# Optimization experiments

Hardware: AMD Instinct MI355X
Metric: run time of the kernel (lower is better)

The kernel has to match this reference:

```python
import jax, jax.numpy as jnp
import numpy as np

RMS_EPS = 1.1920928955078125e-07  # torch.finfo(float32).eps, nn.RMSNorm default when eps=None


def setup_inputs() -> dict:
    key = jax.random.key(0)
    ks = jax.random.split(key, 7)
    B, T, C, Wh, E, K = 8, 4096, 256, 1024, 8, 2
    return {
        "x": jax.random.normal(ks[0], (B, T, C), dtype=jnp.float32),
        "rms_weight": jnp.ones((C,), dtype=jnp.float32),
        "W1": jax.random.normal(ks[1], (E, C, Wh), dtype=jnp.float32),
        "b1": jax.random.normal(ks[2], (E, Wh), dtype=jnp.float32),
        "W2": jax.random.normal(ks[3], (E, Wh, C), dtype=jnp.float32),
        "b2": jax.random.normal(ks[4], (E, C), dtype=jnp.float32),
        "expert_ids": jax.random.randint(ks[5], (B, T, K), 0, E, dtype=jnp.int64),
    }


def reference(x, rms_weight, W1, b1, W2, b2, expert_ids):
    # RMSNorm over last dim (torch nn.RMSNorm, eps = float32 eps)
    xn = x * jax.lax.rsqrt(jnp.mean(x * x, axis=-1, keepdims=True) + RMS_EPS) * rms_weight
    # Per-expert 2-layer MLP. The torch code gathers per-token weight copies then bmm's;
    # mathematically identical (and far cheaper in memory) is: run every expert densely,
    # then gather the K selected expert outputs per token.
    h = jax.nn.gelu(jnp.einsum("btc,ecw->btew", xn, W1) + b1, approximate=False)  # [B,T,E,Wh]
    y = jnp.einsum("btew,ewc->btec", h, W2) + b2  # [B,T,E,C]
    # gather selected experts: [B,T,K,C]; dropout p is 0.0 (eval) -> identity
    out = jnp.take_along_axis(y, expert_ids[..., None], axis=2)
    return out
```

## Files before the change

kernel.cpp:

```cpp
#include <hip/hip_runtime.h>
#include <cstdint>

typedef unsigned short ushort_t;
typedef __bf16 bf16x8 __attribute__((ext_vector_type(8)));
typedef ushort_t u16x8 __attribute__((ext_vector_type(8)));
typedef float f32x4 __attribute__((ext_vector_type(4)));
typedef uint32_t u32x4 __attribute__((ext_vector_type(4)));

#define RMS_EPS 1.1920928955078125e-07f

__device__ __forceinline__ ushort_t f2bf(float f) {
  uint32_t u = __builtin_bit_cast(uint32_t, f);
  u += 0x7fffu + ((u >> 16) & 1u);
  return (ushort_t)(u >> 16);
}

__device__ __forceinline__ void g2l16(const ushort_t* g, ushort_t* l) {
  __builtin_amdgcn_global_load_lds(
      (const __attribute__((address_space(1))) uint32_t*)g,
      (__attribute__((address_space(3))) uint32_t*)l, 16, 0, 0);
}

__device__ __forceinline__ f32x4 mfma32(bf16x8 a, bf16x8 b, f32x4 c) {
  return __builtin_amdgcn_mfma_f32_16x16x32_bf16(a, b, c, 0, 0, 0);
}

__device__ __forceinline__ float gelu1(float v) {
  float v2 = v * v;
  float u_ = (0.044715f * v2) * v + v;
  float tq = __expf(-1.5957691216057308f * u_);
  return v * __builtin_amdgcn_rcpf(1.0f + tq);
}

__global__ void rmsnorm_cast(const float* __restrict__ x, const float* __restrict__ w,
                             ushort_t* __restrict__ xn) {
  int token = blockIdx.x * 4 + (threadIdx.x >> 6);
  int lane = threadIdx.x & 63;
  const float4* row = reinterpret_cast<const float4*>(x + (size_t)token * 256);
  float4 v = row[lane];
  float s = v.x * v.x + v.y * v.y + v.z * v.z + v.w * v.w;
#pragma unroll
  for (int off = 1; off < 64; off <<= 1) s += __shfl_xor(s, off);
  float inv = rsqrtf(s * (1.0f / 256.0f) + RMS_EPS);
  const float4* wr = reinterpret_cast<const float4*>(w);
  float4 wv = wr[lane];
  ushort4 o;
  o.x = f2bf(v.x * inv * wv.x);
  o.y = f2bf(v.y * inv * wv.y);
  o.z = f2bf(v.z * inv * wv.z);
  o.w = f2bf(v.w * inv * wv.w);
  *reinterpret_cast<ushort4*>(xn + (size_t)token * 256 + lane * 4) = o;
}

__global__ __launch_bounds__(256) void pack_w(const float* __restrict__ W1,
                                              const float* __restrict__ W2,
                                              ushort_t* __restrict__ w1f,
                                              ushort_t* __restrict__ w2f) {
  __shared__ ushort_t tile[64][130];
  int b = blockIdx.x;
  int isW2 = b >= 256;
  const float* src; ushort_t* dst; int e, kt, wt, rs;
  if (!isW2) { e = b >> 5; kt = (b >> 3) & 3; wt = b & 7; src = W1; dst = w1f; rs = 1024; }
  else { b -= 256; e = b >> 5; kt = (b >> 1) & 15; wt = b & 1; src = W2; dst = w2f; rs = 256; }
  int k0 = kt * 64, c0 = wt * 128;
  const float* sb = src + ((size_t)e << 18) + (size_t)k0 * rs + c0;
  int t = threadIdx.x;
#pragma unroll
  for (int i = 0; i < 8; ++i) {
    int f = i * 1024 + t * 4;
    int r = f >> 7, c = f & 127;
    float4 v = *reinterpret_cast<const float4*>(sb + (size_t)r * rs + c);
    ushort2 lo, hi;
    lo.x = f2bf(v.x); lo.y = f2bf(v.y); hi.x = f2bf(v.z); hi.y = f2bf(v.w);
    *reinterpret_cast<ushort2*>(&tile[r][c]) = lo;
    *reinterpret_cast<ushort2*>(&tile[r][c + 2]) = hi;
  }
  __syncthreads();
  int lane = t & 63, l16 = lane & 15, quad = lane >> 4;
  int wave = t >> 6;
  if (!isW2) {
#pragma unroll
    for (int p = 0; p < 4; ++p) {
      int u = p * 256 + t;
      int kk2 = (u >> 9) & 1;
      int rr = kk2 * 32 + quad * 8;
      int nt = (u >> 6) & 1, chL = (u >> 7) & 3;
      int cc = chL * 32 + nt * 16 + l16;
      u16x8 o;
#pragma unroll
      for (int j = 0; j < 8; ++j) o[j] = tile[rr + j][cc];
      size_t U = ((size_t)e * 32768) + (size_t)(wt * 4 + chL) * 1024 + (kt * 2 + kk2) * 128 + nt * 64 + lane;
      *reinterpret_cast<u16x8*>(dst + U * 8) = o;
    }
  } else {
#pragma unroll
    for (int p = 0; p < 4; ++p) {
      int u = p * 4 + wave;
      int chL = u >> 3, ctL = u & 7;
      int cc = ctL * 16 + l16;
      u16x8 o;
#pragma unroll
      for (int j = 0; j < 4; ++j) o[j] = tile[chL * 32 + quad * 4 + j][cc];
#pragma unroll
      for (int j = 0; j < 4; ++j) o[4 + j] = tile[chL * 32 + 16 + quad * 4 + j][cc];
      size_t U = (((size_t)(e * 32 + kt * 2 + chL) * 16) + (wt * 8 + ctL)) * 64 + lane;
      *reinterpret_cast<u16x8*>(dst + U * 8) = o;
    }
  }
}

__global__ void route_pairs(const int* __restrict__ eids, int* __restrict__ cnt,
                            int* __restrict__ lists) {
  __shared__ int lcnt[8], lbase[8];
  int tid = threadIdx.x;
  if (tid < 8) lcnt[tid] = 0;
  __syncthreads();
  int p = blockIdx.x * 256 + tid;
  int e = eids[p];
  int lpos = atomicAdd(&lcnt[e], 1);
  __syncthreads();
  if (tid < 8) lbase[tid] = atomicAdd(&cnt[tid], lcnt[tid]);
  __syncthreads();
  lists[e * 65536 + lbase[e] + lpos] = p;
}

__global__ __launch_bounds__(256, 2) void moe_mlp(
    const ushort_t* __restrict__ xn,
    const ushort_t* __restrict__ w1f,
    const ushort_t* __restrict__ w2f,
    const float* __restrict__ b1,
    const float* __restrict__ b2,
    const int* __restrict__ cnt,
    const int* __restrict__ lists,
    float* __restrict__ out)
{
  __shared__ __align__(16) ushort_t w1b[2][8192];
  __shared__ __align__(16) ushort_t w2b[8192];

  int flat = blockIdx.x;
  int e = -1, tile = 0, accum = 0, n_e = 0;
#pragma unroll
  for (int i = 0; i < 8; ++i) {
    int c = cnt[i];
    int t = (c + 127) >> 7;
    if (e < 0 && flat < accum + t) { e = i; tile = flat - accum; n_e = c; }
    accum += t;
  }
  if (e < 0) return;
  int start = tile * 128;

  int tid = threadIdx.x;
  int wave = tid >> 6, lane = tid & 63, l16 = lane & 15, quad = lane >> 4;

  const ushort_t* w1e = w1f + ((size_t)e << 18);
  const ushort_t* w2e = w2f + ((size_t)e << 18);
  const int* le = lists + e * 65536;

  int gi0 = start + wave * 32 + l16;
  int gi1 = gi0 + 16;
  int pr0 = le[(gi0 < n_e) ? gi0 : 0];
  int pr1 = le[(gi1 < n_e) ? gi1 : 0];

#pragma unroll
  for (int j = 0; j < 4; ++j) {
    int p = j * 4 + wave;
    g2l16(w1e + p * 512 + lane * 8, &w1b[0][p * 512]);
  }

  bf16x8 afr[2][8];
  {
    const u32x4* ar0 = reinterpret_cast<const u32x4*>(xn + (size_t)(pr0 >> 1) * 256);
    const u32x4* ar1 = reinterpret_cast<const u32x4*>(xn + (size_t)(pr1 >> 1) * 256);
#pragma unroll
    for (int kk = 0; kk < 8; ++kk) {
      afr[0][kk] = __builtin_bit_cast(bf16x8, ar0[kk * 4 + quad]);
      afr[1][kk] = __builtin_bit_cast(bf16x8, ar1[kk * 4 + quad]);
    }
  }

  f32x4 acc[2][16];
#pragma unroll
  for (int mt = 0; mt < 2; ++mt)
#pragma unroll
    for (int ct = 0; ct < 16; ++ct) acc[mt][ct] = (f32x4){0.f, 0.f, 0.f, 0.f};

  const float* b1e = b1 + e * 1024;

  for (int ch = 0; ch < 32; ++ch) {
    int cur = ch & 1;
    __syncthreads();

    {
      const ushort_t* n2 = w2e + ch * 8192;
#pragma unroll
      for (int j = 0; j < 4; ++j) {
        int p = j * 4 + wave;
        g2l16(n2 + p * 512 + lane * 8, &w2b[p * 512]);
      }
    }
    if (ch + 1 < 32) {
      const ushort_t* n1 = w1e + (ch + 1) * 8192;
#pragma unroll
      for (int j = 0; j < 4; ++j) {
        int p = j * 4 + wave;
        g2l16(n1 + p * 512 + lane * 8, &w1b[cur ^ 1][p * 512]);
      }
    }

    int w0 = ch * 32;
    f32x4 bia0 = *reinterpret_cast<const f32x4*>(b1e + w0 + quad * 4);
    f32x4 bia1 = *reinterpret_cast<const f32x4*>(b1e + w0 + 16 + quad * 4);

    const ushort_t* l1 = w1b[cur];
    f32x4 ht00 = (f32x4){0.f, 0.f, 0.f, 0.f};
    f32x4 ht01 = (f32x4){0.f, 0.f, 0.f, 0.f};
    f32x4 ht10 = (f32x4){0.f, 0.f, 0.f, 0.f};
    f32x4 ht11 = (f32x4){0.f, 0.f, 0.f, 0.f};
#pragma unroll
    for (int kk = 0; kk < 8; ++kk) {
      bf16x8 wA = *reinterpret_cast<const bf16x8*>(l1 + ((kk * 2 + 0) * 64 + lane) * 8);
      bf16x8 wB = *reinterpret_cast<const bf16x8*>(l1 + ((kk * 2 + 1) * 64 + lane) * 8);
      ht00 = mfma32(wA, afr[0][kk], ht00);
      ht10 = mfma32(wA, afr[1][kk], ht10);
      ht01 = mfma32(wB, afr[0][kk], ht01);
      ht11 = mfma32(wB, afr[1][kk], ht11);
    }

    u16x8 hp0, hp1;
#pragma unroll
    for (int r = 0; r < 4; ++r) {
      hp0[r]     = f2bf(gelu1(ht00[r] + bia0[r]));
      hp0[4 + r] = f2bf(gelu1(ht01[r] + bia1[r]));
      hp1[r]     = f2bf(gelu1(ht10[r] + bia0[r]));
      hp1[4 + r] = f2bf(gelu1(ht11[r] + bia1[r]));
    }
    bf16x8 hF0 = __builtin_bit_cast(bf16x8, hp0);
    bf16x8 hF1 = __builtin_bit_cast(bf16x8, hp1);

    __syncthreads();

#pragma unroll
    for (int ct = 0; ct < 16; ++ct) {
      bf16x8 wq = *reinterpret_cast<const bf16x8*>(w2b + (ct * 64 + lane) * 8);
      acc[0][ct] = mfma32(wq, hF0, acc[0][ct]);
      acc[1][ct] = mfma32(wq, hF1, acc[1][ct]);
    }
  }

  const float* b2e = b2 + e * 256;
#pragma unroll
  for (int mt = 0; mt < 2; ++mt) {
    int gi = mt ? gi1 : gi0;
    int pr = mt ? pr1 : pr0;
    if (gi < n_e) {
      float* orow = out + (size_t)pr * 256;
#pragma unroll
      for (int ct = 0; ct < 16; ++ct) {
        f32x4 bv = *reinterpret_cast<const f32x4*>(b2e + ct * 16 + quad * 4);
        f32x4 o = acc[mt][ct] + bv;
        *reinterpret_cast<f32x4*>(orow + ct * 16 + quad * 4) = o;
      }
    }
  }
}

extern "C" void kernel_launch(void* const* d_in, const int* in_sizes, int n_in,
                              void* d_out, int out_size, void* d_ws, size_t ws_size,
                              hipStream_t stream) {
  const float* x  = (const float*)d_in[0];
  const float* rw = (const float*)d_in[1];
  const float* W1 = (const float*)d_in[2];
  const float* b1 = (const float*)d_in[3];
  const float* W2 = (const float*)d_in[4];
  const float* b2 = (const float*)d_in[5];
  const int* eids = (const int*)d_in[6];
  float* out = (float*)d_out;

  char* ws = (char*)d_ws;
  ushort_t* xn  = (ushort_t*)(ws);
  ushort_t* w1f = (ushort_t*)(ws + 16777216);
  ushort_t* w2f = (ushort_t*)(ws + 20971520);
  int* cnt      = (int*)(ws + 25165824);
  int* lists    = (int*)(ws + 25166080);

  hipMemsetAsync(cnt, 0, 8 * sizeof(int), stream);
  rmsnorm_cast<<<8192, 256, 0, stream>>>(x, rw, xn);
  pack_w<<<512, 256, 0, stream>>>(W1, W2, w1f, w2f);
  route_pairs<<<256, 256, 0, stream>>>(eids, cnt, lists);
  moe_mlp<<<519, 256, 0, stream>>>(xn, w1f, w2f, b1, b2, cnt, lists, out);
}
```

Measured before the change: 259.9 us.

## Halve MoE token tile to 64, remap blocks across XCDs, polynomial GELU

Token tiles per block shrink from 128 to 64, so each wave handles one 16-row M tile instead of two. The grid grows to 1032 blocks and launch bounds rise to 3 blocks per CU, trading weight reuse per block for more parallelism and lower register pressure. Block indices are remapped so consecutive tiles, which share expert weights, land on the same XCD for L2 locality. The tanh-form GELU (exp plus reciprocal) is replaced by a clamped odd polynomial erf approximation. This adds approximation error near the clamp and doubles the weight traffic per token.

Result: faster. 224.6 us (-13.6%).

```diff
diff --git a/kernel.cpp b/kernel.cpp
--- a/kernel.cpp
+++ b/kernel.cpp
@@ -26,10 +26,14 @@
 }
 
 __device__ __forceinline__ float gelu1(float v) {
-  float v2 = v * v;
-  float u_ = (0.044715f * v2) * v + v;
-  float tq = __expf(-1.5957691216057308f * u_);
-  return v * __builtin_amdgcn_rcpf(1.0f + tq);
+  float vc = fminf(fmaxf(v, -2.9f), 2.9f);
+  float x2 = vc * vc;
+  float p = fmaf(-0.000414256f, x2, 0.0107517f);
+  p = fmaf(p, x2, -0.1136149f);
+  p = fmaf(p, x2, 0.786301f);
+  float E = vc * p;
+  float t = 0.5f * v;
+  return fmaf(t, E, t);
 }
 
 __global__ void rmsnorm_cast(const float* __restrict__ x, const float* __restrict__ w,
@@ -124,7 +128,7 @@
   lists[e * 65536 + lbase[e] + lpos] = p;
 }
 
-__global__ __launch_bounds__(256, 2) void moe_mlp(
+__global__ __launch_bounds__(256, 3) void moe_mlp(
     const ushort_t* __restrict__ xn,
     const ushort_t* __restrict__ w1f,
     const ushort_t* __restrict__ w2f,
@@ -137,17 +141,21 @@
   __shared__ __align__(16) ushort_t w1b[2][8192];
   __shared__ __align__(16) ushort_t w2b[8192];
 
-  int flat = blockIdx.x;
+  int nwg = gridDim.x;
+  int q = nwg >> 3, r = nwg & 7;
+  int xcd = blockIdx.x & 7, sub = blockIdx.x >> 3;
+  int flat = (xcd < r ? xcd * (q + 1) : r * (q + 1) + (xcd - r) * q) + sub;
+
   int e = -1, tile = 0, accum = 0, n_e = 0;
 #pragma unroll
   for (int i = 0; i < 8; ++i) {
     int c = cnt[i];
-    int t = (c + 127) >> 7;
+    int t = (c + 63) >> 6;
     if (e < 0 && flat < accum + t) { e = i; tile = flat - accum; n_e = c; }
     accum += t;
   }
   if (e < 0) return;
-  int start = tile * 128;
+  int start = tile * 64;
 
   int tid = threadIdx.x;
   int wave = tid >> 6, lane = tid & 63, l16 = lane & 15, quad = lane >> 4;
@@ -156,10 +164,8 @@
   const ushort_t* w2e = w2f + ((size_t)e << 18);
   const int* le = lists + e * 65536;
 
-  int gi0 = start + wave * 32 + l16;
-  int gi1 = gi0 + 16;
-  int pr0 = le[(gi0 < n_e) ? gi0 : 0];
-  int pr1 = le[(gi1 < n_e) ? gi1 : 0];
+  int gi = start + wave * 16 + l16;
+  int pr = le[(gi < n_e) ? gi : 0];
 
 #pragma unroll
   for (int j = 0; j < 4; ++j) {
@@ -167,22 +173,17 @@
     g2l16(w1e + p * 512 + lane * 8, &w1b[0][p * 512]);
   }
 
-  bf16x8 afr[2][8];
+  bf16x8 afr[8];
   {
-    const u32x4* ar0 = reinterpret_cast<const u32x4*>(xn + (size_t)(pr0 >> 1) * 256);
-    const u32x4* ar1 = reinterpret_cast<const u32x4*>(xn + (size_t)(pr1 >> 1) * 256);
-#pragma unroll
-    for (int kk = 0; kk < 8; ++kk) {
-      afr[0][kk] = __builtin_bit_cast(bf16x8, ar0[kk * 4 + quad]);
-      afr[1][kk] = __builtin_bit_cast(bf16x8, ar1[kk * 4 + quad]);
-    }
-  }
-
-  f32x4 acc[2][16];
-#pragma unroll
-  for (int mt = 0; mt < 2; ++mt)
-#pragma unroll
-    for (int ct = 0; ct < 16; ++ct) acc[mt][ct] = (f32x4){0.f, 0.f, 0.f, 0.f};
+    const u32x4* ar = reinterpret_cast<const u32x4*>(xn + (size_t)(pr >> 1) * 256);
+#pragma unroll
+    for (int kk = 0; kk < 8; ++kk)
+      afr[kk] = __builtin_bit_cast(bf16x8, ar[kk * 4 + quad]);
+  }
+
+  f32x4 acc[16];
+#pragma unroll
+  for (int ct = 0; ct < 16; ++ct) acc[ct] = (f32x4){0.f, 0.f, 0.f, 0.f};
 
   const float* b1e = b1 + e * 1024;
 
@@ -212,54 +213,41 @@
     f32x4 bia1 = *reinterpret_cast<const f32x4*>(b1e + w0 + 16 + quad * 4);
 
     const ushort_t* l1 = w1b[cur];
-    f32x4 ht00 = (f32x4){0.f, 0.f, 0.f, 0.f};
-    f32x4 ht01 = (f32x4){0.f, 0.f, 0.f, 0.f};
-    f32x4 ht10 = (f32x4){0.f, 0.f, 0.f, 0.f};
-    f32x4 ht11 = (f32x4){0.f, 0.f, 0.f, 0.f};
+    f32x4 ht0 = (f32x4){0.f, 0.f, 0.f, 0.f};
+    f32x4 ht1 = (f32x4){0.f, 0.f, 0.f, 0.f};
 #pragma unroll
     for (int kk = 0; kk < 8; ++kk) {
       bf16x8 wA = *reinterpret_cast<const bf16x8*>(l1 + ((kk * 2 + 0) * 64 + lane) * 8);
       bf16x8 wB = *reinterpret_cast<const bf16x8*>(l1 + ((kk * 2 + 1) * 64 + lane) * 8);
-      ht00 = mfma32(wA, afr[0][kk], ht00);
-      ht10 = mfma32(wA, afr[1][kk], ht10);
-      ht01 = mfma32(wB, afr[0][kk], ht01);
-      ht11 = mfma32(wB, afr[1][kk], ht11);
-    }
-
-    u16x8 hp0, hp1;
-#pragma unroll
-    for (int r = 0; r < 4; ++r) {
-      hp0[r]     = f2bf(gelu1(ht00[r] + bia0[r]));
-      hp0[4 + r] = f2bf(gelu1(ht01[r] + bia1[r]));
-      hp1[r]     = f2bf(gelu1(ht10[r] + bia0[r]));
-      hp1[4 + r] = f2bf(gelu1(ht11[r] + bia1[r]));
-    }
-    bf16x8 hF0 = __builtin_bit_cast(bf16x8, hp0);
-    bf16x8 hF1 = __builtin_bit_cast(bf16x8, hp1);
+      ht0 = mfma32(wA, afr[kk], ht0);
+      ht1 = mfma32(wB, afr[kk], ht1);
+    }
+
+    u16x8 hp;
+#pragma unroll
+    for (int rr = 0; rr < 4; ++rr) {
+      hp[rr]     = f2bf(gelu1(ht0[rr] + bia0[rr]));
+      hp[4 + rr] = f2bf(gelu1(ht1[rr] + bia1[rr]));
+    }
+    bf16x8 hF = __builtin_bit_cast(bf16x8, hp);
 
     __syncthreads();
 
 #pragma unroll
     for (int ct = 0; ct < 16; ++ct) {
       bf16x8 wq = *reinterpret_cast<const bf16x8*>(w2b + (ct * 64 + lane) * 8);
-      acc[0][ct] = mfma32(wq, hF0, acc[0][ct]);
-      acc[1][ct] = mfma32(wq, hF1, acc[1][ct]);
+      acc[ct] = mfma32(wq, hF, acc[ct]);
     }
   }
 
   const float* b2e = b2 + e * 256;
-#pragma unroll
-  for (int mt = 0; mt < 2; ++mt) {
-    int gi = mt ? gi1 : gi0;
-    int pr = mt ? pr1 : pr0;
-    if (gi < n_e) {
-      float* orow = out + (size_t)pr * 256;
-#pragma unroll
-      for (int ct = 0; ct < 16; ++ct) {
-        f32x4 bv = *reinterpret_cast<const f32x4*>(b2e + ct * 16 + quad * 4);
-        f32x4 o = acc[mt][ct] + bv;
-        *reinterpret_cast<f32x4*>(orow + ct * 16 + quad * 4) = o;
-      }
+  if (gi < n_e) {
+    float* orow = out + (size_t)pr * 256;
+#pragma unroll
+    for (int ct = 0; ct < 16; ++ct) {
+      f32x4 bv = *reinterpret_cast<const f32x4*>(b2e + ct * 16 + quad * 4);
+      f32x4 o = acc[ct] + bv;
+      *reinterpret_cast<f32x4*>(orow + ct * 16 + quad * 4) = o;
     }
   }
 }
@@ -287,5 +275,5 @@
   rmsnorm_cast<<<8192, 256, 0, stream>>>(x, rw, xn);
   pack_w<<<512, 256, 0, stream>>>(W1, W2, w1f, w2f);
   route_pairs<<<256, 256, 0, stream>>>(eids, cnt, lists);
-  moe_mlp<<<519, 256, 0, stream>>>(xn, w1f, w2f, b1, b2, cnt, lists, out);
-}
+  moe_mlp<<<1032, 256, 0, stream>>>(xn, w1f, w2f, b1, b2, cnt, lists, out);
+}
```

## Fuse preprocessing kernels, widen MoE tiles to 256 rows, polynomial GELU

Applied to the files above, without the earlier changes.

Merges the rmsnorm, weight-packing and routing kernels into one launch to cut launch overhead. The MoE kernel moves to 512-thread blocks covering 256 rows per tile, so each staged weight chunk is shared by twice as many rows. Blocks are interleaved across experts. GELU becomes a clamped odd polynomial in place of the exp-based form, trading some accuracy for fewer instructions. Token-pair indices are reloaded at store time to save registers.

New measurement: 291.4 us. +12.1%, slower.

```diff
diff --git a/kernel.cpp b/kernel.cpp
--- a/kernel.cpp
+++ b/kernel.cpp
@@ -26,105 +26,109 @@
 }
 
 __device__ __forceinline__ float gelu1(float v) {
-  float v2 = v * v;
-  float u_ = (0.044715f * v2) * v + v;
-  float tq = __expf(-1.5957691216057308f * u_);
-  return v * __builtin_amdgcn_rcpf(1.0f + tq);
-}
-
-__global__ void rmsnorm_cast(const float* __restrict__ x, const float* __restrict__ w,
-                             ushort_t* __restrict__ xn) {
-  int token = blockIdx.x * 4 + (threadIdx.x >> 6);
-  int lane = threadIdx.x & 63;
-  const float4* row = reinterpret_cast<const float4*>(x + (size_t)token * 256);
-  float4 v = row[lane];
-  float s = v.x * v.x + v.y * v.y + v.z * v.z + v.w * v.w;
-#pragma unroll
-  for (int off = 1; off < 64; off <<= 1) s += __shfl_xor(s, off);
-  float inv = rsqrtf(s * (1.0f / 256.0f) + RMS_EPS);
-  const float4* wr = reinterpret_cast<const float4*>(w);
-  float4 wv = wr[lane];
-  ushort4 o;
-  o.x = f2bf(v.x * inv * wv.x);
-  o.y = f2bf(v.y * inv * wv.y);
-  o.z = f2bf(v.z * inv * wv.z);
-  o.w = f2bf(v.w * inv * wv.w);
-  *reinterpret_cast<ushort4*>(xn + (size_t)token * 256 + lane * 4) = o;
-}
-
-__global__ __launch_bounds__(256) void pack_w(const float* __restrict__ W1,
-                                              const float* __restrict__ W2,
-                                              ushort_t* __restrict__ w1f,
-                                              ushort_t* __restrict__ w2f) {
+  float vc = fminf(fmaxf(v, -2.9f), 2.9f);
+  float x2 = vc * vc;
+  float p = fmaf(-0.000414256f, x2, 0.0107517f);
+  p = fmaf(p, x2, -0.1136149f);
+  p = fmaf(p, x2, 0.786301f);
+  float E = vc * p;
+  float t = 0.5f * v;
+  return fmaf(t, E, t);
+}
+
+__global__ __launch_bounds__(256) void fused_pre(
+    const float* __restrict__ x, const float* __restrict__ rw,
+    ushort_t* __restrict__ xn,
+    const float* __restrict__ W1, const float* __restrict__ W2,
+    ushort_t* __restrict__ w1f, ushort_t* __restrict__ w2f,
+    const int* __restrict__ eids, int* __restrict__ cnt,
+    int* __restrict__ lists) {
   __shared__ ushort_t tile[64][130];
-  int b = blockIdx.x;
-  int isW2 = b >= 256;
-  const float* src; ushort_t* dst; int e, kt, wt, rs;
-  if (!isW2) { e = b >> 5; kt = (b >> 3) & 3; wt = b & 7; src = W1; dst = w1f; rs = 1024; }
-  else { b -= 256; e = b >> 5; kt = (b >> 1) & 15; wt = b & 1; src = W2; dst = w2f; rs = 256; }
-  int k0 = kt * 64, c0 = wt * 128;
-  const float* sb = src + ((size_t)e << 18) + (size_t)k0 * rs + c0;
+  __shared__ int lcnt[8], lbase[8];
+  int bid = blockIdx.x;
   int t = threadIdx.x;
-#pragma unroll
-  for (int i = 0; i < 8; ++i) {
-    int f = i * 1024 + t * 4;
-    int r = f >> 7, c = f & 127;
-    float4 v = *reinterpret_cast<const float4*>(sb + (size_t)r * rs + c);
-    ushort2 lo, hi;
-    lo.x = f2bf(v.x); lo.y = f2bf(v.y); hi.x = f2bf(v.z); hi.y = f2bf(v.w);
-    *reinterpret_cast<ushort2*>(&tile[r][c]) = lo;
-    *reinterpret_cast<ushort2*>(&tile[r][c + 2]) = hi;
-  }
-  __syncthreads();
-  int lane = t & 63, l16 = lane & 15, quad = lane >> 4;
-  int wave = t >> 6;
-  if (!isW2) {
-#pragma unroll
-    for (int p = 0; p < 4; ++p) {
-      int u = p * 256 + t;
-      int kk2 = (u >> 9) & 1;
-      int rr = kk2 * 32 + quad * 8;
-      int nt = (u >> 6) & 1, chL = (u >> 7) & 3;
-      int cc = chL * 32 + nt * 16 + l16;
-      u16x8 o;
-#pragma unroll
-      for (int j = 0; j < 8; ++j) o[j] = tile[rr + j][cc];
-      size_t U = ((size_t)e * 32768) + (size_t)(wt * 4 + chL) * 1024 + (kt * 2 + kk2) * 128 + nt * 64 + lane;
-      *reinterpret_cast<u16x8*>(dst + U * 8) = o;
+
+  if (bid < 8192) {
+    int token = bid * 4 + (t >> 6);
+    int lane = t & 63;
+    const float4* row = reinterpret_cast<const float4*>(x + (size_t)token * 256);
+    float4 v = row[lane];
+    float s = v.x * v.x + v.y * v.y + v.z * v.z + v.w * v.w;
+#pragma unroll
+    for (int off = 1; off < 64; off <<= 1) s += __shfl_xor(s, off);
+    float inv = rsqrtf(s * (1.0f / 256.0f) + RMS_EPS);
+    const float4* wr = reinterpret_cast<const float4*>(rw);
+    float4 wv = wr[lane];
+    ushort4 o;
+    o.x = f2bf(v.x * inv * wv.x);
+    o.y = f2bf(v.y * inv * wv.y);
+    o.z = f2bf(v.z * inv * wv.z);
+    o.w = f2bf(v.w * inv * wv.w);
+    *reinterpret_cast<ushort4*>(xn + (size_t)token * 256 + lane * 4) = o;
+  } else if (bid < 8704) {
+    int b = bid - 8192;
+    int isW2 = b >= 256;
+    const float* src; ushort_t* dst; int e, kt, wt, rs;
+    if (!isW2) { e = b >> 5; kt = (b >> 3) & 3; wt = b & 7; src = W1; dst = w1f; rs = 1024; }
+    else { b -= 256; e = b >> 5; kt = (b >> 1) & 15; wt = b & 1; src = W2; dst = w2f; rs = 256; }
+    int k0 = kt * 64, c0 = wt * 128;
+    const float* sb = src + ((size_t)e << 18) + (size_t)k0 * rs + c0;
+#pragma unroll
+    for (int i = 0; i < 8; ++i) {
+      int f = i * 1024 + t * 4;
+      int r = f >> 7, c = f & 127;
+      float4 v = *reinterpret_cast<const float4*>(sb + (size_t)r * rs + c);
+      ushort2 lo, hi;
+      lo.x = f2bf(v.x); lo.y = f2bf(v.y); hi.x = f2bf(v.z); hi.y = f2bf(v.w);
+      *reinterpret_cast<ushort2*>(&tile[r][c]) = lo;
+      *reinterpret_cast<ushort2*>(&tile[r][c + 2]) = hi;
+    }
+    __syncthreads();
+    int lane = t & 63, l16 = lane & 15, quad = lane >> 4;
+    int wave = t >> 6;
+    if (!isW2) {
+#pragma unroll
+      for (int p = 0; p < 4; ++p) {
+        int u = p * 256 + t;
+        int kk2 = (u >> 9) & 1;
+        int rr = kk2 * 32 + quad * 8;
+        int nt = (u >> 6) & 1, chL = (u >> 7) & 3;
+        int cc = chL * 32 + nt * 16 + l16;
+        u16x8 o;
+#pragma unroll
+        for (int j = 0; j < 8; ++j) o[j] = tile[rr + j][cc];
+        size_t U = ((size_t)e * 32768) + (size_t)(wt * 4 + chL) * 1024 + (kt * 2 + kk2) * 128 + nt * 64 + lane;
+        *reinterpret_cast<u16x8*>(dst + U * 8) = o;
+      }
+    } else {
+#pragma unroll
+      for (int p = 0; p < 4; ++p) {
+        int u = p * 4 + wave;
+        int chL = u >> 3, ctL = u & 7;
+        int cc = ctL * 16 + l16;
+        u16x8 o;
+#pragma unroll
+        for (int j = 0; j < 4; ++j) o[j] = tile[chL * 32 + quad * 4 + j][cc];
+#pragma unroll
+        for (int j = 0; j < 4; ++j) o[4 + j] = tile[chL * 32 + 16 + quad * 4 + j][cc];
+        size_t U = (((size_t)(e * 32 + kt * 2 + chL) * 16) + (wt * 8 + ctL)) * 64 + lane;
+        *reinterpret_cast<u16x8*>(dst + U * 8) = o;
+      }
     }
   } else {
-#pragma unroll
-    for (int p = 0; p < 4; ++p) {
-      int u = p * 4 + wave;
-      int chL = u >> 3, ctL = u & 7;
-      int cc = ctL * 16 + l16;
-      u16x8 o;
-#pragma unroll
-      for (int j = 0; j < 4; ++j) o[j] = tile[chL * 32 + quad * 4 + j][cc];
-#pragma unroll
-      for (int j = 0; j < 4; ++j) o[4 + j] = tile[chL * 32 + 16 + quad * 4 + j][cc];
-      size_t U = (((size_t)(e * 32 + kt * 2 + chL) * 16) + (wt * 8 + ctL)) * 64 + lane;
-      *reinterpret_cast<u16x8*>(dst + U * 8) = o;
-    }
-  }
-}
-
-__global__ void route_pairs(const int* __restrict__ eids, int* __restrict__ cnt,
-                            int* __restrict__ lists) {
-  __shared__ int lcnt[8], lbase[8];
-  int tid = threadIdx.x;
-  if (tid < 8) lcnt[tid] = 0;
-  __syncthreads();
-  int p = blockIdx.x * 256 + tid;
-  int e = eids[p];
-  int lpos = atomicAdd(&lcnt[e], 1);
-  __syncthreads();
-  if (tid < 8) lbase[tid] = atomicAdd(&cnt[tid], lcnt[tid]);
-  __syncthreads();
-  lists[e * 65536 + lbase[e] + lpos] = p;
-}
-
-__global__ __launch_bounds__(256, 2) void moe_mlp(
+    if (t < 8) lcnt[t] = 0;
+    __syncthreads();
+    int p = (bid - 8704) * 256 + t;
+    int e = eids[p];
+    int lpos = atomicAdd(&lcnt[e], 1);
+    __syncthreads();
+    if (t < 8) lbase[t] = atomicAdd(&cnt[t], lcnt[t]);
+    __syncthreads();
+    lists[e * 65536 + lbase[e] + lpos] = p;
+  }
+}
+
+__global__ __launch_bounds__(512, 2) void moe_mlp(
     const ushort_t* __restrict__ xn,
     const ushort_t* __restrict__ w1f,
     const ushort_t* __restrict__ w2f,
@@ -137,17 +141,19 @@
   __shared__ __align__(16) ushort_t w1b[2][8192];
   __shared__ __align__(16) ushort_t w2b[8192];
 
-  int flat = blockIdx.x;
+  int cpx = gridDim.x >> 3;
+  int flat = (blockIdx.x & 7) * cpx + (blockIdx.x >> 3);
+
   int e = -1, tile = 0, accum = 0, n_e = 0;
 #pragma unroll
   for (int i = 0; i < 8; ++i) {
     int c = cnt[i];
-    int t = (c + 127) >> 7;
-    if (e < 0 && flat < accum + t) { e = i; tile = flat - accum; n_e = c; }
-    accum += t;
+    int ti = (c + 255) >> 8;
+    if (e < 0 && flat < accum + ti) { e = i; tile = flat - accum; n_e = c; }
+    accum += ti;
   }
   if (e < 0) return;
-  int start = tile * 128;
+  int start = tile * 256;
 
   int tid = threadIdx.x;
   int wave = tid >> 6, lane = tid & 63, l16 = lane & 15, quad = lane >> 4;
@@ -156,19 +162,17 @@
   const ushort_t* w2e = w2f + ((size_t)e << 18);
   const int* le = lists + e * 65536;
 
-  int gi0 = start + wave * 32 + l16;
-  int gi1 = gi0 + 16;
-  int pr0 = le[(gi0 < n_e) ? gi0 : 0];
-  int pr1 = le[(gi1 < n_e) ? gi1 : 0];
-
-#pragma unroll
-  for (int j = 0; j < 4; ++j) {
-    int p = j * 4 + wave;
+#pragma unroll
+  for (int j = 0; j < 2; ++j) {
+    int p = j * 8 + wave;
     g2l16(w1e + p * 512 + lane * 8, &w1b[0][p * 512]);
   }
 
   bf16x8 afr[2][8];
   {
+    int gi0 = start + wave * 32 + l16;
+    int pr0 = le[(gi0 < n_e) ? gi0 : 0];
+    int pr1 = le[(gi0 + 16 < n_e) ? gi0 + 16 : 0];
     const u32x4* ar0 = reinterpret_cast<const u32x4*>(xn + (size_t)(pr0 >> 1) * 256);
     const u32x4* ar1 = reinterpret_cast<const u32x4*>(xn + (size_t)(pr1 >> 1) * 256);
 #pragma unroll
@@ -193,23 +197,19 @@
     {
       const ushort_t* n2 = w2e + ch * 8192;
 #pragma unroll
-      for (int j = 0; j < 4; ++j) {
-        int p = j * 4 + wave;
+      for (int j = 0; j < 2; ++j) {
+        int p = j * 8 + wave;
         g2l16(n2 + p * 512 + lane * 8, &w2b[p * 512]);
       }
     }
     if (ch + 1 < 32) {
       const ushort_t* n1 = w1e + (ch + 1) * 8192;
 #pragma unroll
-      for (int j = 0; j < 4; ++j) {
-        int p = j * 4 + wave;
+      for (int j = 0; j < 2; ++j) {
+        int p = j * 8 + wave;
         g2l16(n1 + p * 512 + lane * 8, &w1b[cur ^ 1][p * 512]);
       }
     }
-
-    int w0 = ch * 32;
-    f32x4 bia0 = *reinterpret_cast<const f32x4*>(b1e + w0 + quad * 4);
-    f32x4 bia1 = *reinterpret_cast<const f32x4*>(b1e + w0 + 16 + quad * 4);
 
     const ushort_t* l1 = w1b[cur];
     f32x4 ht00 = (f32x4){0.f, 0.f, 0.f, 0.f};
@@ -226,13 +226,17 @@
       ht11 = mfma32(wB, afr[1][kk], ht11);
     }
 
+    int w0 = ch * 32;
+    f32x4 bia0 = *reinterpret_cast<const f32x4*>(b1e + w0 + quad * 4);
+    f32x4 bia1 = *reinterpret_cast<const f32x4*>(b1e + w0 + 16 + quad * 4);
+
     u16x8 hp0, hp1;
 #pragma unroll
-    for (int r = 0; r < 4; ++r) {
-      hp0[r]     = f2bf(gelu1(ht00[r] + bia0[r]));
-      hp0[4 + r] = f2bf(gelu1(ht01[r] + bia1[r]));
-      hp1[r]     = f2bf(gelu1(ht10[r] + bia0[r]));
-      hp1[4 + r] = f2bf(gelu1(ht11[r] + bia1[r]));
+    for (int rr = 0; rr < 4; ++rr) {
+      hp0[rr]     = f2bf(gelu1(ht00[rr] + bia0[rr]));
+      hp0[4 + rr] = f2bf(gelu1(ht01[rr] + bia1[rr]));
+      hp1[rr]     = f2bf(gelu1(ht10[rr] + bia0[rr]));
+      hp1[4 + rr] = f2bf(gelu1(ht11[rr] + bia1[rr]));
     }
     bf16x8 hF0 = __builtin_bit_cast(bf16x8, hp0);
     bf16x8 hF1 = __builtin_bit_cast(bf16x8, hp1);
@@ -250,9 +254,9 @@
   const float* b2e = b2 + e * 256;
 #pragma unroll
   for (int mt = 0; mt < 2; ++mt) {
-    int gi = mt ? gi1 : gi0;
-    int pr = mt ? pr1 : pr0;
+    int gi = start + wave * 32 + mt * 16 + l16;
     if (gi < n_e) {
+      int pr = le[gi];
       float* orow = out + (size_t)pr * 256;
 #pragma unroll
       for (int ct = 0; ct < 16; ++ct) {
@@ -284,8 +288,6 @@
   int* lists    = (int*)(ws + 25166080);
 
   hipMemsetAsync(cnt, 0, 8 * sizeof(int), stream);
-  rmsnorm_cast<<<8192, 256, 0, stream>>>(x, rw, xn);
-  pack_w<<<512, 256, 0, stream>>>(W1, W2, w1f, w2f);
-  route_pairs<<<256, 256, 0, stream>>>(eids, cnt, lists);
-  moe_mlp<<<519, 256, 0, stream>>>(xn, w1f, w2f, b1, b2, cnt, lists, out);
-}
+  fused_pre<<<8960, 256, 0, stream>>>(x, rw, xn, W1, W2, w1f, w2f, eids, cnt, lists);
+  moe_mlp<<<264, 512, 0, stream>>>(xn, w1f, w2f, b1, b2, cnt, lists, out);
+}
```
